# Kernel optimization log

Hardware: AMD Instinct MI355X
Metric: run time of the kernel (lower is better)

Reference implementation:

```python
import jax, jax.numpy as jnp
import numpy as np

D_MODEL = 1024
N_HEADS = 16
D_K = D_MODEL // N_HEADS


def setup_inputs() -> dict:
    key = jax.random.key(0)
    ks = jax.random.split(key, 12)
    B, S = 2, 2048
    scale = 1.0 / np.sqrt(D_MODEL)
    inp = {
        "q": jax.random.normal(ks[0], (B, S, D_MODEL), jnp.float32),
        "k": jax.random.normal(ks[1], (B, S, D_MODEL), jnp.float32),
        "v": jax.random.normal(ks[2], (B, S, D_MODEL), jnp.float32),
        "Wq": jax.random.normal(ks[3], (D_MODEL, D_MODEL), jnp.float32) * scale,
        "bq": jnp.zeros((D_MODEL,), jnp.float32),
        "Wk": jax.random.normal(ks[4], (D_MODEL, D_MODEL), jnp.float32) * scale,
        "bk": jnp.zeros((D_MODEL,), jnp.float32),
        "Wv": jax.random.normal(ks[5], (D_MODEL, D_MODEL), jnp.float32) * scale,
        "bv": jnp.zeros((D_MODEL,), jnp.float32),
        "Wo": jax.random.normal(ks[6], (D_MODEL, D_MODEL), jnp.float32) * scale,
        "bo": jnp.zeros((D_MODEL,), jnp.float32),
    }
    return inp


def reference(q, k, v, Wq, bq, Wk, bk, Wv, bv, Wo, bo):
    B, S, _ = q.shape
    # QKV projections, split into heads: [B, H, S, d_k]
    def proj(x, W, b):
        y = x @ W.T + b
        return y.reshape(B, -1, N_HEADS, D_K).transpose(0, 2, 1, 3)

    qh = proj(q, Wq, bq)
    kh = proj(k, Wk, bk)
    vh = proj(v, Wv, bv)

    scores = jnp.einsum("bhqd,bhkd->bhqk", qh, kh) / jnp.sqrt(
        jnp.asarray(D_K, qh.dtype)
    )
    attention = jax.nn.softmax(scores, axis=-1)  # dropout is identity in eval
    out = jnp.einsum("bhqk,bhkd->bhqd", attention, vh)
    out = out.transpose(0, 2, 1, 3).reshape(B, -1, N_HEADS * D_K)
    out = out @ Wo.T + bo
    return (out, attention)
```

## Files before the change

kernel.cpp:

```cpp
#include <hip/hip_runtime.h>

typedef __attribute__((ext_vector_type(4))) float f32x4;
typedef __attribute__((ext_vector_type(4))) unsigned short u16x4;
typedef __attribute__((ext_vector_type(8))) unsigned short u16x8;
typedef __attribute__((ext_vector_type(8))) short short8;
typedef __attribute__((ext_vector_type(4))) unsigned int u32x4;

#define DEVFN static __device__ __forceinline__

DEVFN unsigned short f2bf(float f) {
    union { float f; unsigned int u; } v; v.f = f;
    unsigned int r = v.u + 0x7FFFu + ((v.u >> 16) & 1u);
    return (unsigned short)(r >> 16);
}

DEVFN f32x4 mfma16(short8 a, short8 b, f32x4 c) {
    return __builtin_amdgcn_mfma_f32_16x16x32_bf16(a, b, c, 0, 0, 0);
}


__global__ __launch_bounds__(256) void cvt_w4(
    const float* __restrict__ w0, const float* __restrict__ w1,
    const float* __restrict__ w2, const float* __restrict__ w3,
    unsigned short* __restrict__ d0, unsigned short* __restrict__ d1,
    unsigned short* __restrict__ d2, unsigned short* __restrict__ d3) {
    const int z = blockIdx.y;
    const float* s = (z == 0) ? w0 : (z == 1) ? w1 : (z == 2) ? w2 : w3;
    unsigned short* d = (z == 0) ? d0 : (z == 1) ? d1 : (z == 2) ? d2 : d3;
    int i = (blockIdx.x * 256 + threadIdx.x) * 4;
    f32x4 v = *(const f32x4*)(s + i);
    u16x4 o;
    o[0] = f2bf(v[0]); o[1] = f2bf(v[1]); o[2] = f2bf(v[2]); o[3] = f2bf(v[3]);
    *(u16x4*)(d + i) = o;
}

__global__ __launch_bounds__(256) void qkv_gemm(
    const float* __restrict__ q, const float* __restrict__ k, const float* __restrict__ v,
    const unsigned short* __restrict__ Wqb, const unsigned short* __restrict__ Wkb,
    const unsigned short* __restrict__ Wvb,
    const float* __restrict__ bq, const float* __restrict__ bk, const float* __restrict__ bv,
    unsigned short* __restrict__ qh, unsigned short* __restrict__ kh,
    unsigned short* __restrict__ vt)
{
    constexpr int AS = 40;
    __shared__ __attribute__((aligned(16))) unsigned short Asm[128 * AS];
    __shared__ __attribute__((aligned(16))) unsigned short Bsm[128 * AS];

    const int z = blockIdx.y;
    const float* X = (z == 0) ? q : (z == 1) ? k : v;
    const unsigned short* W = (z == 0) ? Wqb : (z == 1) ? Wkb : Wvb;
    const float* bias = (z == 0) ? bq : (z == 1) ? bk : bv;

    const int bid0 = blockIdx.x;
    const int swz = (bid0 & 7) * 32 + (bid0 >> 3);
    const int bm = swz >> 3, bn = swz & 7;

    const int tid = threadIdx.x;
    const int lane = tid & 63, wid = tid >> 6;
    const int wm = wid >> 1, wn = wid & 1;
    const int lg = lane >> 4, lr = lane & 15;

    f32x4 acc[4][4] = {};

    const float* Xb = X + (size_t)(bm * 128) * 1024;
    const unsigned short* Wb = W + (size_t)(bn * 128) * 1024;
    const int ar = tid >> 3, ac = (tid & 7) * 4;
    const int br = tid >> 2, bc = (tid & 3) * 8;

    for (int kt = 0; kt < 32; ++kt) {
        __syncthreads();
        #pragma unroll
        for (int s4 = 0; s4 < 4; ++s4) {
            int row = s4 * 32 + ar;
            f32x4 xv = *(const f32x4*)(Xb + (size_t)row * 1024 + kt * 32 + ac);
            u16x4 pk;
            pk[0] = f2bf(xv[0]); pk[1] = f2bf(xv[1]);
            pk[2] = f2bf(xv[2]); pk[3] = f2bf(xv[3]);
            *(u16x4*)(&Asm[row * AS + ac]) = pk;
        }
        #pragma unroll
        for (int s2 = 0; s2 < 2; ++s2) {
            int row = s2 * 64 + br;
            *(u16x8*)(&Bsm[row * AS + bc]) =
                *(const u16x8*)(Wb + (size_t)row * 1024 + kt * 32 + bc);
        }
        __syncthreads();

        short8 af[4], bf[4];
        #pragma unroll
        for (int i = 0; i < 4; i++)
            af[i] = *(const short8*)(&Asm[(wm * 64 + i * 16 + lr) * AS + lg * 8]);
        #pragma unroll
        for (int j = 0; j < 4; j++)
            bf[j] = *(const short8*)(&Bsm[(wn * 64 + j * 16 + lr) * AS + lg * 8]);

        if (z != 2) {
            #pragma unroll
            for (int i = 0; i < 4; i++)
                #pragma unroll
                for (int j = 0; j < 4; j++)
                    acc[i][j] = mfma16(af[i], bf[j], acc[i][j]);
        } else {
            #pragma unroll
            for (int i = 0; i < 4; i++)
                #pragma unroll
                for (int j = 0; j < 4; j++)
                    acc[i][j] = mfma16(bf[i], af[j], acc[i][j]);
        }
    }

    if (z != 2) {
        unsigned short* Y = (z == 0) ? qh : kh;
        #pragma unroll
        for (int i = 0; i < 4; i++) {
            int mrow = bm * 128 + wm * 64 + i * 16 + lg * 4;
            #pragma unroll
            for (int j = 0; j < 4; j++) {
                int ncol = bn * 128 + wn * 64 + j * 16 + lr;
                float bb = bias[ncol];
                #pragma unroll
                for (int ii = 0; ii < 4; ii++)
                    Y[(size_t)(mrow + ii) * 1024 + ncol] = f2bf(acc[i][j][ii] + bb);
            }
        }
    } else {
        #pragma unroll
        for (int i = 0; i < 4; i++) {
            int nrow0 = bn * 128 + wn * 64 + i * 16 + lg * 4;
            #pragma unroll
            for (int j = 0; j < 4; j++) {
                int mcol = bm * 128 + wm * 64 + j * 16 + lr;
                int b_ = mcol >> 11, s_ = mcol & 2047;
                #pragma unroll
                for (int ii = 0; ii < 4; ii++) {
                    int nrow = nrow0 + ii;
                    float val = acc[i][j][ii] + bias[nrow];
                    int h_ = nrow >> 6, d_ = nrow & 63;
                    vt[(size_t)((b_ * 16 + h_) * 64 + d_) * 2048 + s_] = f2bf(val);
                }
            }
        }
    }
}

__global__ __launch_bounds__(256) void attn_fused(
    const unsigned short* __restrict__ qh,
    const unsigned short* __restrict__ kh,
    const unsigned short* __restrict__ vt,
    float* __restrict__ attn_out, unsigned short* __restrict__ ctx)
{
    __shared__ float Lsm[4][16];
    __shared__ float Om[3][1024];

    const int bid = blockIdx.x;
    const int swz = (bid & 7) * 512 + (bid >> 3);
    const int bh = swz >> 7, qt = swz & 127;
    const int b = bh >> 4, h = bh & 15;
    const int tid = threadIdx.x, ks = tid >> 6, lane = tid & 63;
    const int lg = lane >> 4, lr = lane & 15;
    const int qbase = qt * 16;

    const unsigned short* Qrow = qh + (size_t)(b * 2048 + qbase + lr) * 1024 + h * 64;
    short8 bq0 = *(const short8*)(Qrow + lg * 8);
    short8 bq1 = *(const short8*)(Qrow + 32 + lg * 8);

    const unsigned short* Kbase = kh + (size_t)(b * 2048 + ks * 512) * 1024 + h * 64;
    const unsigned short* Vbase = vt + (size_t)(bh * 64) * 2048 + ks * 512;

    const int a0 = lg & 1;
    const bool bswap = (lg == 1) || (lg == 2);

    unsigned int paw[8][8];
    float lsum = 0.f;

    #pragma unroll
    for (int kt = 0; kt < 8; ++kt) {
        f32x4 sc[4] = {};
        const unsigned short* Kt = Kbase + (size_t)(kt * 64) * 1024;
        #pragma unroll
        for (int c = 0; c < 4; c++) {
            const unsigned short* Kr = Kt + (size_t)(c * 16 + lr) * 1024 + lg * 8;
            sc[c] = mfma16(*(const short8*)(Kr), bq0, sc[c]);
            sc[c] = mfma16(*(const short8*)(Kr + 32), bq1, sc[c]);
        }
        float p[4][4];
        #pragma unroll
        for (int c = 0; c < 4; c++)
            #pragma unroll
            for (int i = 0; i < 4; i++) {
                p[c][i] = __expf(sc[c][i] * 0.125f);
                lsum += p[c][i];
            }

        unsigned int w32[4][2];
        #pragma unroll
        for (int c = 0; c < 4; c++)
            #pragma unroll
            for (int w = 0; w < 2; w++)
                asm("v_cvt_pk_bf16_f32 %0, %1, %2"
                    : "=v"(w32[c][w]) : "v"(p[c][2 * w]), "v"(p[c][2 * w + 1]));

        unsigned int Av[2][2][2];
        #pragma unroll
        for (int t = 0; t < 2; t++)
            #pragma unroll
            for (int w = 0; w < 2; w++) {
                unsigned int keep = a0 ? w32[2 * t + 1][w] : w32[2 * t][w];
                unsigned int snd  = a0 ? w32[2 * t][w]     : w32[2 * t + 1][w];
                unsigned int rcv = __shfl_xor(snd, 16, 64);
                Av[t][0][w] = a0 ? rcv : keep;
                Av[t][1][w] = a0 ? keep : rcv;
            }
        #pragma unroll
        for (int t = 0; t < 2; t++)
            #pragma unroll
            for (int s = 0; s < 2; s++)
                #pragma unroll
                for (int w = 0; w < 2; w++) {
                    unsigned int sw = __shfl_xor(Av[t][s][w], 48, 64);
                    paw[kt][t * 4 + s * 2 + w] = bswap ? sw : Av[t][s][w];
                }
    }

    lsum += __shfl_xor(lsum, 16, 64);
    lsum += __shfl_xor(lsum, 32, 64);
    if (lg == 0) Lsm[ks][lr] = lsum;
    __syncthreads();
    const float il = 1.0f / (Lsm[0][lr] + Lsm[1][lr] + Lsm[2][lr] + Lsm[3][lr]);

    float* prow = attn_out + (size_t)(bh * 2048 + qbase + lr) * 2048 + ks * 512;
    f32x4 o[4] = {};
    #pragma unroll
    for (int kt = 0; kt < 8; ++kt) {
        float sl[8], sh[8];
        unsigned int s32[8];
        #pragma unroll
        for (int r = 0; r < 8; r++) {
            unsigned int u = paw[kt][r];
            float lo = __uint_as_float(u << 16) * il;
            float hi = __uint_as_float(u & 0xFFFF0000u) * il;
            sl[r] = lo; sh[r] = hi;
            asm("v_cvt_pk_bf16_f32 %0, %1, %2" : "=v"(s32[r]) : "v"(lo), "v"(hi));
        }
        float* pk = prow + kt * 64 + lg * 8;
        f32x4 st0 = { sl[0], sh[0], sl[1], sh[1] };
        f32x4 st1 = { sl[2], sh[2], sl[3], sh[3] };
        f32x4 st2 = { sl[4], sh[4], sl[5], sh[5] };
        f32x4 st3 = { sl[6], sh[6], sl[7], sh[7] };
        __builtin_nontemporal_store(st0, (f32x4*)(pk));
        __builtin_nontemporal_store(st1, (f32x4*)(pk + 4));
        __builtin_nontemporal_store(st2, (f32x4*)(pk + 32));
        __builtin_nontemporal_store(st3, (f32x4*)(pk + 36));

        u32x4 w0 = { s32[0], s32[1], s32[2], s32[3] };
        u32x4 w1 = { s32[4], s32[5], s32[6], s32[7] };
        short8 pa0 = *(short8*)&w0;
        short8 pa1 = *(short8*)&w1;

        const unsigned short* Vt = Vbase + kt * 64;
        #pragma unroll
        for (int g = 0; g < 4; g++) {
            const unsigned short* Vr = Vt + (size_t)(g * 16 + lr) * 2048 + lg * 8;
            o[g] = mfma16(pa0, *(const short8*)(Vr), o[g]);
            o[g] = mfma16(pa1, *(const short8*)(Vr + 32), o[g]);
        }
    }

    __syncthreads();
    if (ks != 0) {
        float* Ob = &Om[ks - 1][0];
        #pragma unroll
        for (int g = 0; g < 4; g++)
            #pragma unroll
            for (int i = 0; i < 4; i++)
                Ob[(lg * 4 + i) * 64 + g * 16 + lr] = o[g][i];
    }
    __syncthreads();
    if (ks == 0) {
        #pragma unroll
        for (int g = 0; g < 4; g++)
            #pragma unroll
            for (int i = 0; i < 4; i++) {
                int idx = (lg * 4 + i) * 64 + g * 16 + lr;
                float val = o[g][i] + Om[0][idx] + Om[1][idx] + Om[2][idx];
                int qrow = qbase + lg * 4 + i;
                int dcol = h * 64 + g * 16 + lr;
                ctx[(size_t)(b * 2048 + qrow) * 1024 + dcol] = f2bf(val);
            }
    }
}

__global__ __launch_bounds__(256) void out_gemm(
    const unsigned short* __restrict__ ctx, const unsigned short* __restrict__ Wob,
    const float* __restrict__ bo, float* __restrict__ out)
{
    constexpr int AS = 40;
    __shared__ __attribute__((aligned(16))) unsigned short Asm[128 * AS];
    __shared__ __attribute__((aligned(16))) unsigned short Bsm[128 * AS];

    const int bid0 = blockIdx.x;
    const int swz = (bid0 & 7) * 32 + (bid0 >> 3);
    const int bm = swz >> 3, bn = swz & 7;
    const int tid = threadIdx.x;
    const int lane = tid & 63, wid = tid >> 6;
    const int wm = wid >> 1, wn = wid & 1;
    const int lg = lane >> 4, lr = lane & 15;

    f32x4 acc[4][4] = {};

    const unsigned short* Ab = ctx + (size_t)(bm * 128) * 1024;
    const unsigned short* Wb = Wob + (size_t)(bn * 128) * 1024;
    const int br = tid >> 2, bc = (tid & 3) * 8;

    for (int kt = 0; kt < 32; ++kt) {
        __syncthreads();
        #pragma unroll
        for (int s2 = 0; s2 < 2; ++s2) {
            int row = s2 * 64 + br;
            *(u16x8*)(&Asm[row * AS + bc]) =
                *(const u16x8*)(Ab + (size_t)row * 1024 + kt * 32 + bc);
            *(u16x8*)(&Bsm[row * AS + bc]) =
                *(const u16x8*)(Wb + (size_t)row * 1024 + kt * 32 + bc);
        }
        __syncthreads();

        short8 af[4], bf[4];
        #pragma unroll
        for (int i = 0; i < 4; i++)
            af[i] = *(const short8*)(&Asm[(wm * 64 + i * 16 + lr) * AS + lg * 8]);
        #pragma unroll
        for (int j = 0; j < 4; j++)
            bf[j] = *(const short8*)(&Bsm[(wn * 64 + j * 16 + lr) * AS + lg * 8]);
        #pragma unroll
        for (int i = 0; i < 4; i++)
            #pragma unroll
            for (int j = 0; j < 4; j++)
                acc[i][j] = mfma16(af[i], bf[j], acc[i][j]);
    }

    #pragma unroll
    for (int i = 0; i < 4; i++) {
        int mrow = bm * 128 + wm * 64 + i * 16 + lg * 4;
        #pragma unroll
        for (int j = 0; j < 4; j++) {
            int ncol = bn * 128 + wn * 64 + j * 16 + lr;
            float bb = bo[ncol];
            #pragma unroll
            for (int ii = 0; ii < 4; ii++)
                out[(size_t)(mrow + ii) * 1024 + ncol] = acc[i][j][ii] + bb;
        }
    }
}

extern "C" void kernel_launch(void* const* d_in, const int* in_sizes, int n_in,
                              void* d_out, int out_size, void* d_ws, size_t ws_size,
                              hipStream_t stream) {
    const float* q  = (const float*)d_in[0];
    const float* k  = (const float*)d_in[1];
    const float* v  = (const float*)d_in[2];
    const float* Wq = (const float*)d_in[3];
    const float* bq = (const float*)d_in[4];
    const float* Wk = (const float*)d_in[5];
    const float* bk = (const float*)d_in[6];
    const float* Wv = (const float*)d_in[7];
    const float* bv = (const float*)d_in[8];
    const float* Wo = (const float*)d_in[9];
    const float* bo = (const float*)d_in[10];

    float* out  = (float*)d_out;
    float* attn = out + (size_t)4096 * 1024;

    unsigned short* wsp = (unsigned short*)d_ws;
    unsigned short* Wqb = wsp;
    unsigned short* Wkb = wsp + (size_t)(1 << 20);
    unsigned short* Wvb = wsp + (size_t)2 * (1 << 20);
    unsigned short* Wob = wsp + (size_t)3 * (1 << 20);
    unsigned short* qh  = wsp + (size_t)4 * (1 << 20);
    unsigned short* kh  = wsp + (size_t)8 * (1 << 20);
    unsigned short* vt  = wsp + (size_t)12 * (1 << 20);
    unsigned short* ctx = wsp + (size_t)16 * (1 << 20);

    cvt_w4<<<dim3(1024, 4), 256, 0, stream>>>(Wq, Wk, Wv, Wo, Wqb, Wkb, Wvb, Wob);

    qkv_gemm<<<dim3(256, 3), 256, 0, stream>>>(q, k, v, Wqb, Wkb, Wvb,
                                               bq, bk, bv, qh, kh, vt);

    attn_fused<<<4096, 256, 0, stream>>>(qh, kh, vt, attn, ctx);

    out_gemm<<<256, 256, 0, stream>>>(ctx, Wob, bo, out);
}
```

Before: 417.8 us.

## Split attention key range across eight waves and defer softmax normalization of PV

Each attention block now runs eight waves, each covering 256 keys instead of 512, halving per-wave register state (paw array) and raising parallelism per query tile. The PV product now uses unnormalized bf16 exponentials directly, dropping the per-element renormalize-and-repack step, and the normalization is applied once when the eight partial outputs are reduced. That reduction is spread across all waves, each handling two query rows. The cost is more shared memory (32 KB for partial outputs) and more barrier and reduction work.

```diff
diff --git a/kernel.cpp b/kernel.cpp
--- a/kernel.cpp
+++ b/kernel.cpp
@@ -143,14 +143,14 @@
     }
 }
 
-__global__ __launch_bounds__(256) void attn_fused(
+__global__ __launch_bounds__(512, 4) void attn_fused(
     const unsigned short* __restrict__ qh,
     const unsigned short* __restrict__ kh,
     const unsigned short* __restrict__ vt,
     float* __restrict__ attn_out, unsigned short* __restrict__ ctx)
 {
-    __shared__ float Lsm[4][16];
-    __shared__ float Om[3][1024];
+    __shared__ float Lsm[8][16];
+    __shared__ float Om[8][1024];
 
     const int bid = blockIdx.x;
     const int swz = (bid & 7) * 512 + (bid >> 3);
@@ -164,17 +164,17 @@
     short8 bq0 = *(const short8*)(Qrow + lg * 8);
     short8 bq1 = *(const short8*)(Qrow + 32 + lg * 8);
 
-    const unsigned short* Kbase = kh + (size_t)(b * 2048 + ks * 512) * 1024 + h * 64;
-    const unsigned short* Vbase = vt + (size_t)(bh * 64) * 2048 + ks * 512;
+    const unsigned short* Kbase = kh + (size_t)(b * 2048 + ks * 256) * 1024 + h * 64;
+    const unsigned short* Vbase = vt + (size_t)(bh * 64) * 2048 + ks * 256;
 
     const int a0 = lg & 1;
     const bool bswap = (lg == 1) || (lg == 2);
 
-    unsigned int paw[8][8];
+    unsigned int paw[4][8];
     float lsum = 0.f;
 
     #pragma unroll
-    for (int kt = 0; kt < 8; ++kt) {
+    for (int kt = 0; kt < 4; ++kt) {
         f32x4 sc[4] = {};
         const unsigned short* Kt = Kbase + (size_t)(kt * 64) * 1024;
         #pragma unroll
@@ -226,21 +226,21 @@
     lsum += __shfl_xor(lsum, 32, 64);
     if (lg == 0) Lsm[ks][lr] = lsum;
     __syncthreads();
-    const float il = 1.0f / (Lsm[0][lr] + Lsm[1][lr] + Lsm[2][lr] + Lsm[3][lr]);
-
-    float* prow = attn_out + (size_t)(bh * 2048 + qbase + lr) * 2048 + ks * 512;
+    float Lt = 0.f;
+    #pragma unroll
+    for (int w = 0; w < 8; w++) Lt += Lsm[w][lr];
+    const float il = 1.0f / Lt;
+
+    float* prow = attn_out + (size_t)(bh * 2048 + qbase + lr) * 2048 + ks * 256;
     f32x4 o[4] = {};
     #pragma unroll
-    for (int kt = 0; kt < 8; ++kt) {
+    for (int kt = 0; kt < 4; ++kt) {
         float sl[8], sh[8];
-        unsigned int s32[8];
         #pragma unroll
         for (int r = 0; r < 8; r++) {
             unsigned int u = paw[kt][r];
-            float lo = __uint_as_float(u << 16) * il;
-            float hi = __uint_as_float(u & 0xFFFF0000u) * il;
-            sl[r] = lo; sh[r] = hi;
-            asm("v_cvt_pk_bf16_f32 %0, %1, %2" : "=v"(s32[r]) : "v"(lo), "v"(hi));
+            sl[r] = __uint_as_float(u << 16) * il;
+            sh[r] = __uint_as_float(u & 0xFFFF0000u) * il;
         }
         float* pk = prow + kt * 64 + lg * 8;
         f32x4 st0 = { sl[0], sh[0], sl[1], sh[1] };
@@ -252,8 +252,8 @@
         __builtin_nontemporal_store(st2, (f32x4*)(pk + 32));
         __builtin_nontemporal_store(st3, (f32x4*)(pk + 36));
 
-        u32x4 w0 = { s32[0], s32[1], s32[2], s32[3] };
-        u32x4 w1 = { s32[4], s32[5], s32[6], s32[7] };
+        u32x4 w0 = { paw[kt][0], paw[kt][1], paw[kt][2], paw[kt][3] };
+        u32x4 w1 = { paw[kt][4], paw[kt][5], paw[kt][6], paw[kt][7] };
         short8 pa0 = *(short8*)&w0;
         short8 pa1 = *(short8*)&w1;
 
@@ -267,8 +267,8 @@
     }
 
     __syncthreads();
-    if (ks != 0) {
-        float* Ob = &Om[ks - 1][0];
+    {
+        float* Ob = &Om[ks][0];
         #pragma unroll
         for (int g = 0; g < 4; g++)
             #pragma unroll
@@ -276,17 +276,16 @@
                 Ob[(lg * 4 + i) * 64 + g * 16 + lr] = o[g][i];
     }
     __syncthreads();
-    if (ks == 0) {
-        #pragma unroll
-        for (int g = 0; g < 4; g++)
-            #pragma unroll
-            for (int i = 0; i < 4; i++) {
-                int idx = (lg * 4 + i) * 64 + g * 16 + lr;
-                float val = o[g][i] + Om[0][idx] + Om[1][idx] + Om[2][idx];
-                int qrow = qbase + lg * 4 + i;
-                int dcol = h * 64 + g * 16 + lr;
-                ctx[(size_t)(b * 2048 + qrow) * 1024 + dcol] = f2bf(val);
-            }
+    #pragma unroll
+    for (int rr = 0; rr < 2; rr++) {
+        int r = ks * 2 + rr;
+        float Ls = 0.f;
+        #pragma unroll
+        for (int w = 0; w < 8; w++) Ls += Lsm[w][r];
+        float s = 0.f;
+        #pragma unroll
+        for (int w = 0; w < 8; w++) s += Om[w][r * 64 + lane];
+        ctx[(size_t)(b * 2048 + qbase + r) * 1024 + h * 64 + lane] = f2bf(s / Ls);
     }
 }
 
@@ -385,7 +384,7 @@
     qkv_gemm<<<dim3(256, 3), 256, 0, stream>>>(q, k, v, Wqb, Wkb, Wvb,
                                                bq, bk, bv, qh, kh, vt);
 
-    attn_fused<<<4096, 256, 0, stream>>>(qh, kh, vt, attn, ctx);
+    attn_fused<<<4096, 512, 0, stream>>>(qh, kh, vt, attn, ctx);
 
     out_gemm<<<256, 256, 0, stream>>>(ctx, Wob, bo, out);
 }
```

New measurement: 422.0 us. About the same (+1.0%).
